# Performance work log

Hardware: AMD Instinct MI355X
Metric: run time of the kernel (lower is better)

The kernel has to match this reference:

```python
import jax, jax.numpy as jnp
import numpy as np


def setup_inputs() -> dict:
    key = jax.random.key(0)
    k1, k2, k3, k4 = jax.random.split(key, 4)
    in_features, out_features = 4096, 4096
    x = jax.random.normal(k1, (8, 2048, in_features), dtype=jnp.float32)
    # stored in float32 (torch.randint with dtype=float32) holding int values in [-128, 127)
    int8_weights = jax.random.randint(k2, (out_features, in_features), -128, 127).astype(jnp.float32)
    scales = jax.random.normal(k3, (out_features, 1), dtype=jnp.float32)
    zero_point = jnp.zeros((out_features, 1), dtype=jnp.float32)
    bias = jax.random.normal(k4, (1, out_features), dtype=jnp.float32)
    return {"x": x, "int8_weights": int8_weights, "scales": scales,
            "zero_point": zero_point, "bias": bias}


def reference(x, int8_weights, scales, zero_point, bias):
    # affine dequant: per-output-row scale/zero_point -> fp32 weights [out, in]
    w = (int8_weights - zero_point) * scales
    # F.linear: x @ w.T, then add bias
    out = jnp.einsum('bsi,oi->bso', x, w) + bias
    return out
```

## Files before the change

### kernel.cpp

```cpp
#include <hip/hip_runtime.h>


typedef __attribute__((ext_vector_type(8))) short short8;
typedef __attribute__((ext_vector_type(4))) float f32x4;

__device__ __forceinline__ unsigned short f2bf(float f) {
    union { float f; unsigned u; } v; v.f = f;
    unsigned r = v.u + 0x7fffu + ((v.u >> 16) & 1u);
    return (unsigned short)(r >> 16);
}

__device__ __forceinline__ void gl_lds16(const void* g, void* l) {
    __builtin_amdgcn_global_load_lds(
        (const __attribute__((address_space(1))) void*)g,
        (__attribute__((address_space(3))) void*)l, 16, 0, 0);
}

__global__ __launch_bounds__(256)
void cvt_f32_bf16(const float* __restrict__ s, unsigned short* __restrict__ d, size_t n) {
    size_t i = ((size_t)blockIdx.x * 256 + threadIdx.x) * 8;
    if (i >= n) return;
    float4 a = *(const float4*)(s + i);
    float4 b = *(const float4*)(s + i + 4);
    short8 p;
    p[0] = (short)f2bf(a.x); p[1] = (short)f2bf(a.y);
    p[2] = (short)f2bf(a.z); p[3] = (short)f2bf(a.w);
    p[4] = (short)f2bf(b.x); p[5] = (short)f2bf(b.y);
    p[6] = (short)f2bf(b.z); p[7] = (short)f2bf(b.w);
    *(short8*)(d + i) = p;
}

__global__ __launch_bounds__(256, 2)
void w8a16_gemm_sync(const float* __restrict__ Af, const float* __restrict__ Bf,
                     const float* __restrict__ scales, const float* __restrict__ bias,
                     float* __restrict__ C, int M, int N, int K)
{
    __shared__ unsigned short As[128 * 32];
    __shared__ unsigned short Bs[128 * 32];
    const int tid  = threadIdx.x;
    const int lane = tid & 63;
    const int wave = tid >> 6;
    const int l16  = lane & 15;
    const int quad = lane >> 4;
    const int bm   = blockIdx.y;
    const int bn   = blockIdx.x;
    const int wm   = (wave >> 1) * 64;
    const int wn   = (wave & 1) * 64;

    f32x4 acc[4][4];
#pragma unroll
    for (int i = 0; i < 4; ++i)
#pragma unroll
        for (int j = 0; j < 4; ++j)
            acc[i][j] = (f32x4){0.f, 0.f, 0.f, 0.f};

    for (int k0 = 0; k0 < K; k0 += 32) {
#pragma unroll
        for (int it = 0; it < 2; ++it) {
            const int id = it * 256 + tid;
            const int r = id >> 2, s = id & 3;
            const float* sp = Af + (size_t)(bm * 128 + r) * K + k0 + s * 8;
            float4 v0 = *(const float4*)sp;
            float4 v1 = *(const float4*)(sp + 4);
            short8 p;
            p[0] = (short)f2bf(v0.x); p[1] = (short)f2bf(v0.y);
            p[2] = (short)f2bf(v0.z); p[3] = (short)f2bf(v0.w);
            p[4] = (short)f2bf(v1.x); p[5] = (short)f2bf(v1.y);
            p[6] = (short)f2bf(v1.z); p[7] = (short)f2bf(v1.w);
            *(short8*)(&As[id * 8]) = p;
        }
#pragma unroll
        for (int it = 0; it < 2; ++it) {
            const int id = it * 256 + tid;
            const int r = id >> 2, s = id & 3;
            const float* sp = Bf + (size_t)(bn * 128 + r) * K + k0 + s * 8;
            float4 v0 = *(const float4*)sp;
            float4 v1 = *(const float4*)(sp + 4);
            short8 p;
            p[0] = (short)f2bf(v0.x); p[1] = (short)f2bf(v0.y);
            p[2] = (short)f2bf(v0.z); p[3] = (short)f2bf(v0.w);
            p[4] = (short)f2bf(v1.x); p[5] = (short)f2bf(v1.y);
            p[6] = (short)f2bf(v1.z); p[7] = (short)f2bf(v1.w);
            *(short8*)(&Bs[id * 8]) = p;
        }
        __syncthreads();
        short8 af[4], bfr[4];
#pragma unroll
        for (int i = 0; i < 4; ++i)
            af[i] = *(const short8*)(&As[(wm + i * 16 + l16) * 32 + quad * 8]);
#pragma unroll
        for (int j = 0; j < 4; ++j)
            bfr[j] = *(const short8*)(&Bs[(wn + j * 16 + l16) * 32 + quad * 8]);
#pragma unroll
        for (int i = 0; i < 4; ++i)
#pragma unroll
            for (int j = 0; j < 4; ++j)
                acc[i][j] = __builtin_amdgcn_mfma_f32_16x16x32_bf16(
                    af[i], bfr[j], acc[i][j], 0, 0, 0);
        __syncthreads();
    }
#pragma unroll
    for (int j = 0; j < 4; ++j) {
        const int n = bn * 128 + wn + j * 16 + l16;
        const float sc = scales[n];
        const float bi = bias[n];
#pragma unroll
        for (int i = 0; i < 4; ++i) {
            const int mrow = bm * 128 + wm + i * 16 + quad * 4;
#pragma unroll
            for (int r = 0; r < 4; ++r)
                C[(size_t)(mrow + r) * N + n] = acc[i][j][r] * sc + bi;
        }
    }
}

#define BM 256
#define BN 256
#define BK 64

__device__ __forceinline__ int swz(int o) { return o ^ (((o >> 8) & 3) << 4); }

#define LDA(BUF, MI, KS) \
    (*(const short8*)((const char*)&As[0][0] + (BUF) * 32768 + \
        swz((KS) * 16384 + (wr * 128 + (MI) * 16 + l16) * 64 + quad * 16)))
#define LDB(BUF, NI, KS) \
    (*(const short8*)((const char*)&Bs[0][0] + (BUF) * 32768 + \
        swz((KS) * 16384 + (wc * 64 + (NI) * 16 + l16) * 64 + quad * 16)))

#define STAGE_A(BUF, KTID, H) do { \
    const unsigned short* _g = Abase + (size_t)(H) * 128 * K + (KTID) * BK; \
    char* _l = AsL0 + (BUF) * 32768 + (H) * 8192; \
    gl_lds16(_g, _l); \
    gl_lds16(_g + 32, _l + 16384); \
} while (0)
#define STAGE_B(BUF, KTID, H) do { \
    const unsigned short* _g = Bbase + (size_t)(H) * 128 * K + (KTID) * BK; \
    char* _l = BsL0 + (BUF) * 32768 + (H) * 8192; \
    gl_lds16(_g, _l); \
    gl_lds16(_g + 32, _l + 16384); \
} while (0)

#define PHASE(BUF, Q, VMQ, ...) do { \
    short8 a00 = LDA(BUF, 2*(Q),   0); \
    short8 a01 = LDA(BUF, 2*(Q),   1); \
    short8 a10 = LDA(BUF, 2*(Q)+1, 0); \
    short8 a11 = LDA(BUF, 2*(Q)+1, 1); \
    if ((Q) == 0) { \
        _Pragma("unroll") \
        for (int ni = 0; ni < 4; ++ni) { \
            bfr[ni][0] = LDB(BUF, ni, 0); \
            bfr[ni][1] = LDB(BUF, ni, 1); \
        } \
    } \
    __VA_ARGS__; \
    __builtin_amdgcn_s_barrier(); \
    asm volatile("s_waitcnt lgkmcnt(0)" ::: "memory"); \
    __builtin_amdgcn_s_setprio(1); \
    _Pragma("unroll") \
    for (int ni = 0; ni < 4; ++ni) { \
        acc[2*(Q)][ni]   = __builtin_amdgcn_mfma_f32_16x16x32_bf16(a00, bfr[ni][0], acc[2*(Q)][ni],   0, 0, 0); \
        acc[2*(Q)+1][ni] = __builtin_amdgcn_mfma_f32_16x16x32_bf16(a10, bfr[ni][0], acc[2*(Q)+1][ni], 0, 0, 0); \
    } \
    _Pragma("unroll") \
    for (int ni = 0; ni < 4; ++ni) { \
        acc[2*(Q)][ni]   = __builtin_amdgcn_mfma_f32_16x16x32_bf16(a01, bfr[ni][1], acc[2*(Q)][ni],   0, 0, 0); \
        acc[2*(Q)+1][ni] = __builtin_amdgcn_mfma_f32_16x16x32_bf16(a11, bfr[ni][1], acc[2*(Q)+1][ni], 0, 0, 0); \
    } \
    __builtin_amdgcn_s_setprio(0); \
    if (VMQ) { asm volatile("s_waitcnt vmcnt(4)" ::: "memory"); } \
    __builtin_amdgcn_s_barrier(); \
} while (0)

__global__ __launch_bounds__(512, 2)
void w8a16_256(const unsigned short* __restrict__ A, const unsigned short* __restrict__ B,
               const float* __restrict__ scales, const float* __restrict__ bias,
               float* __restrict__ C, int M, int N, int K)
{
    __shared__ unsigned short As[2][BM * BK];
    __shared__ unsigned short Bs[2][BN * BK];

    const int tid  = threadIdx.x;
    const int lane = tid & 63;
    const int w    = tid >> 6;
    const int l16  = lane & 15;
    const int quad = lane >> 4;
    const int wr   = w >> 2;
    const int wc   = w & 3;

    const int mt = M / BM, nt = N / BN;
    const int nwg = mt * nt;
    int id = blockIdx.x;
    if ((nwg & 7) == 0) id = (id & 7) * (nwg >> 3) + (id >> 3);
    const int bm = id % mt;
    const int bn = id / mt;

    const int c4   = (lane & 3) ^ ((lane >> 4) & 3);
    const int srow = w * 16 + (lane >> 2);
    const unsigned short* Abase = A + (size_t)(bm * BM + srow) * K + c4 * 8;
    const unsigned short* Bbase = B + (size_t)(bn * BN + srow) * K + c4 * 8;
    char* AsL0 = (char*)&As[0][0] + w * 1024;
    char* BsL0 = (char*)&Bs[0][0] + w * 1024;

    STAGE_A(0, 0, 0); STAGE_A(0, 0, 1);
    STAGE_B(0, 0, 0); STAGE_B(0, 0, 1);
    STAGE_B(1, 1, 0); STAGE_B(1, 1, 1);

    f32x4 acc[8][4];
#pragma unroll
    for (int i = 0; i < 8; ++i)
#pragma unroll
        for (int j = 0; j < 4; ++j)
            acc[i][j] = (f32x4){0.f, 0.f, 0.f, 0.f};
    short8 bfr[4][2];

    asm volatile("s_waitcnt vmcnt(4)" ::: "memory");
    __builtin_amdgcn_s_barrier();

    const int KT  = K / BK;
    const int NIT = KT / 2;
#pragma unroll 1
    for (int it = 0; it < NIT; ++it) {
        const int g0 = 2 * it;
        const int tA1 = (g0 + 1 < KT) ? g0 + 1 : KT - 1;
        const int tB2 = (g0 + 2 < KT) ? g0 + 2 : KT - 1;
        const int tA2 = (g0 + 2 < KT) ? g0 + 2 : KT - 1;
        const int tB3 = (g0 + 3 < KT) ? g0 + 3 : KT - 1;

        PHASE(0, 0, 0, STAGE_A(1, tA1, 0); STAGE_A(1, tA1, 1));
        PHASE(0, 1, 0, STAGE_B(0, tB2, 0));
        PHASE(0, 2, 0, STAGE_B(0, tB2, 1));
        PHASE(0, 3, 1, (void)0);
        PHASE(1, 0, 0, STAGE_A(0, tA2, 0); STAGE_A(0, tA2, 1));
        PHASE(1, 1, 0, STAGE_B(1, tB3, 0));
        PHASE(1, 2, 0, STAGE_B(1, tB3, 1));
        PHASE(1, 3, 1, (void)0);
    }

#pragma unroll
    for (int ni = 0; ni < 4; ++ni) {
        const int n = bn * BN + wc * 64 + ni * 16 + l16;
        const float sc = scales[n];
        const float bi = bias[n];
#pragma unroll
        for (int mi = 0; mi < 8; ++mi) {
            const size_t r0 = (size_t)(bm * BM + wr * 128 + mi * 16 + quad * 4) * N + n;
#pragma unroll
            for (int r = 0; r < 4; ++r)
                C[r0 + (size_t)r * N] = acc[mi][ni][r] * sc + bi;
        }
    }
}

extern "C" void kernel_launch(void* const* d_in, const int* in_sizes, int n_in,
                              void* d_out, int out_size, void* d_ws, size_t ws_size,
                              hipStream_t stream) {
    const float* x      = (const float*)d_in[0];
    const float* wgt    = (const float*)d_in[1];
    const float* scales = (const float*)d_in[2];
    const float* bias   = (const float*)d_in[4];
    float* out = (float*)d_out;

    const int N = in_sizes[2];
    const int K = in_sizes[1] / N;
    const int M = in_sizes[0] / K;

    const size_t needB = (size_t)N * K * 2;
    const size_t needA = (size_t)M * K * 2;
    const bool fast = (ws_size >= needB + needA) &&
                      (M % BM == 0) && (N % BN == 0) && (K % (2 * BK) == 0);

    if (fast) {
        unsigned short* wB = (unsigned short*)d_ws;
        unsigned short* xB = (unsigned short*)((char*)d_ws + needB);
        size_t nw = (size_t)N * K;
        size_t nx = (size_t)M * K;
        cvt_f32_bf16<<<(unsigned)((nw / 8 + 255) / 256), 256, 0, stream>>>(wgt, wB, nw);
        cvt_f32_bf16<<<(unsigned)((nx / 8 + 255) / 256), 256, 0, stream>>>(x, xB, nx);
        dim3 grid((unsigned)((M / BM) * (N / BN)));
        w8a16_256<<<grid, 512, 0, stream>>>(xB, wB, scales, bias, out, M, N, K);
    } else {
        dim3 grid(N / 128, M / 128);
        w8a16_gemm_sync<<<grid, 256, 0, stream>>>(x, wgt, scales, bias, out, M, N, K);
    }
}
```

Baseline: 987.9 us.

## Merge conversion kernels into one grid-stride launch and retune LDS swizzle

Replaces the two separate fp32-to-bf16 conversion launches with a single grid-stride kernel over a fixed 2048-block grid that handles both the weights and the activations. It also changes the LDS XOR swizzle (bits 7-8 instead of 8-9) and the matching staging column permutation, aiming to reduce LDS bank conflicts on fragment reads. The fallback kernel is refactored to use a shared cvt8 helper. The swizzle change must stay consistent between the write and read sides, otherwise results are wrong.

```diff
diff --git a/kernel.cpp b/kernel.cpp
--- a/kernel.cpp
+++ b/kernel.cpp
@@ -16,18 +16,27 @@
         (__attribute__((address_space(3))) void*)l, 16, 0, 0);
 }
 
-__global__ __launch_bounds__(256)
-void cvt_f32_bf16(const float* __restrict__ s, unsigned short* __restrict__ d, size_t n) {
-    size_t i = ((size_t)blockIdx.x * 256 + threadIdx.x) * 8;
-    if (i >= n) return;
-    float4 a = *(const float4*)(s + i);
-    float4 b = *(const float4*)(s + i + 4);
+__device__ __forceinline__ void cvt8(const float* __restrict__ s,
+                                     unsigned short* __restrict__ d) {
+    float4 a = *(const float4*)s;
+    float4 b = *(const float4*)(s + 4);
     short8 p;
     p[0] = (short)f2bf(a.x); p[1] = (short)f2bf(a.y);
     p[2] = (short)f2bf(a.z); p[3] = (short)f2bf(a.w);
     p[4] = (short)f2bf(b.x); p[5] = (short)f2bf(b.y);
     p[6] = (short)f2bf(b.z); p[7] = (short)f2bf(b.w);
-    *(short8*)(d + i) = p;
+    *(short8*)d = p;
+}
+
+__global__ __launch_bounds__(256)
+void cvt2_f32_bf16(const float* __restrict__ w, unsigned short* __restrict__ wB, size_t cw,
+                   const float* __restrict__ x, unsigned short* __restrict__ xB, size_t cx)
+{
+    const size_t step = (size_t)gridDim.x * 256;
+    for (size_t c = (size_t)blockIdx.x * 256 + threadIdx.x; c < cw + cx; c += step) {
+        if (c < cw) cvt8(w + c * 8, wB + c * 8);
+        else        cvt8(x + (c - cw) * 8, xB + (c - cw) * 8);
+    }
 }
 
 __global__ __launch_bounds__(256, 2)
@@ -59,29 +68,13 @@
         for (int it = 0; it < 2; ++it) {
             const int id = it * 256 + tid;
             const int r = id >> 2, s = id & 3;
-            const float* sp = Af + (size_t)(bm * 128 + r) * K + k0 + s * 8;
-            float4 v0 = *(const float4*)sp;
-            float4 v1 = *(const float4*)(sp + 4);
-            short8 p;
-            p[0] = (short)f2bf(v0.x); p[1] = (short)f2bf(v0.y);
-            p[2] = (short)f2bf(v0.z); p[3] = (short)f2bf(v0.w);
-            p[4] = (short)f2bf(v1.x); p[5] = (short)f2bf(v1.y);
-            p[6] = (short)f2bf(v1.z); p[7] = (short)f2bf(v1.w);
-            *(short8*)(&As[id * 8]) = p;
+            cvt8(Af + (size_t)(bm * 128 + r) * K + k0 + s * 8, &As[id * 8]);
         }
 #pragma unroll
         for (int it = 0; it < 2; ++it) {
             const int id = it * 256 + tid;
             const int r = id >> 2, s = id & 3;
-            const float* sp = Bf + (size_t)(bn * 128 + r) * K + k0 + s * 8;
-            float4 v0 = *(const float4*)sp;
-            float4 v1 = *(const float4*)(sp + 4);
-            short8 p;
-            p[0] = (short)f2bf(v0.x); p[1] = (short)f2bf(v0.y);
-            p[2] = (short)f2bf(v0.z); p[3] = (short)f2bf(v0.w);
-            p[4] = (short)f2bf(v1.x); p[5] = (short)f2bf(v1.y);
-            p[6] = (short)f2bf(v1.z); p[7] = (short)f2bf(v1.w);
-            *(short8*)(&Bs[id * 8]) = p;
+            cvt8(Bf + (size_t)(bn * 128 + r) * K + k0 + s * 8, &Bs[id * 8]);
         }
         __syncthreads();
         short8 af[4], bfr[4];
@@ -118,7 +111,7 @@
 #define BN 256
 #define BK 64
 
-__device__ __forceinline__ int swz(int o) { return o ^ (((o >> 8) & 3) << 4); }
+__device__ __forceinline__ int swz(int o) { return o ^ (((o >> 7) & 3) << 4); }
 
 #define LDA(BUF, MI, KS) \
     (*(const short8*)((const char*)&As[0][0] + (BUF) * 32768 + \
@@ -194,7 +187,7 @@
     const int bm = id % mt;
     const int bn = id / mt;
 
-    const int c4   = (lane & 3) ^ ((lane >> 4) & 3);
+    const int c4   = (lane & 3) ^ ((lane >> 3) & 3);
     const int srow = w * 16 + (lane >> 2);
     const unsigned short* Abase = A + (size_t)(bm * BM + srow) * K + c4 * 8;
     const unsigned short* Bbase = B + (size_t)(bn * BN + srow) * K + c4 * 8;
@@ -267,15 +260,15 @@
     const size_t needB = (size_t)N * K * 2;
     const size_t needA = (size_t)M * K * 2;
     const bool fast = (ws_size >= needB + needA) &&
-                      (M % BM == 0) && (N % BN == 0) && (K % (2 * BK) == 0);
+                      (M % BM == 0) && (N % BN == 0) && (K % (2 * BK) == 0) &&
+                      (K % 8 == 0);
 
     if (fast) {
         unsigned short* wB = (unsigned short*)d_ws;
         unsigned short* xB = (unsigned short*)((char*)d_ws + needB);
-        size_t nw = (size_t)N * K;
-        size_t nx = (size_t)M * K;
-        cvt_f32_bf16<<<(unsigned)((nw / 8 + 255) / 256), 256, 0, stream>>>(wgt, wB, nw);
-        cvt_f32_bf16<<<(unsigned)((nx / 8 + 255) / 256), 256, 0, stream>>>(x, xB, nx);
+        const size_t cw = (size_t)N * K / 8;
+        const size_t cx = (size_t)M * K / 8;
+        cvt2_f32_bf16<<<2048, 256, 0, stream>>>(wgt, wB, cw, x, xB, cx);
         dim3 grid((unsigned)((M / BM) * (N / BN)));
         w8a16_256<<<grid, 512, 0, stream>>>(xB, wB, scales, bias, out, M, N, K);
     } else {
```

After: 978.0 us. About the same (-1.0%).
